# Kernel tuning notes

Hardware: AMD Instinct MI355X
Metric: run time of the kernel (lower is better)

The kernel has to match this reference:

```python
import jax, jax.numpy as jnp
import numpy as np

TOP_K = 2
NEG_INF = -1e30


def setup_inputs() -> dict:
    key = jax.random.key(0)
    ks = jax.random.split(key, 9)
    S, B, D, H, E, O = 2, 2048, 1024, 2048, 8, 1024
    return {
        "xs": jax.random.normal(ks[0], (S, B, D), jnp.float32),
        "Wg": jax.random.normal(ks[1], (D, E), jnp.float32),
        "b": jax.random.normal(ks[2], (E,), jnp.float32),
        "fc1_w": jax.random.normal(ks[3], (E, H, D), jnp.float32) * 0.02,
        "fc1_b": jax.random.normal(ks[4], (E, H), jnp.float32) * 0.02,
        "fc2_w": jax.random.normal(ks[5], (E, H, H), jnp.float32) * 0.02,
        "fc2_b": jax.random.normal(ks[6], (E, H), jnp.float32) * 0.02,
        "final_w": jax.random.normal(ks[7], (O, H), jnp.float32) * 0.02,
        "final_b": jax.random.normal(ks[8], (O,), jnp.float32) * 0.02,
    }


def reference(xs, Wg, b, fc1_w, fc1_b, fc2_w, fc2_b, final_w, final_b):
    # xs: [S, B, D] stacked x_list
    S = xs.shape[0]
    # gate logits H: [S, B, E]
    Hg = jnp.einsum('sbd,de->sbe', xs, Wg) + b
    expert_probs = jax.nn.softmax(Hg, axis=-1)  # per-view full softmax
    # top-k threshold mask (H >= kth largest value)
    topk_vals = jax.lax.top_k(Hg, TOP_K)[0]          # [S, B, K]
    thr = topk_vals[..., -1:]                         # [S, B, 1]
    H_masked = jnp.where(Hg >= thr, Hg, NEG_INF)
    G = jax.nn.softmax(H_masked, axis=-1)             # [S, B, E]
    # dense all-expert FFN: [S, B, E, H]
    h = jnp.einsum('sbd,ehd->sbeh', xs, fc1_w) + fc1_b
    h = jax.nn.relu(h)
    eo = jnp.einsum('sbeh,egh->sbeg', h, fc2_w) + fc2_b
    # gated sum over experts, averaged over views: [B, H]
    combined = jnp.einsum('sbe,sbeh->bh', G, eo) / S
    out = combined @ final_w.T + final_b               # [B, O]
    return out, expert_probs
```

## Files before the change

### kernel.cpp

```cpp
#include <hip/hip_runtime.h>
#include <stdint.h>

#define S_DIM 2
#define B_DIM 2048
#define D_DIM 1024
#define H_DIM 2048
#define E_DIM 8
#define O_DIM 1024
#define NTOK 4096
#define CAP 12288

typedef __attribute__((ext_vector_type(8))) short bf16x8;
typedef __attribute__((ext_vector_type(4))) float f32x4;

__device__ __forceinline__ unsigned short f2bf(float f) {
    union { float f; uint32_t i; } c; c.f = f;
    uint32_t r = c.i + 0x7FFFu + ((c.i >> 16) & 1u);
    return (unsigned short)(r >> 16);
}
__device__ __forceinline__ float bf2f(unsigned short u) {
    union { uint32_t i; float f; } c; c.i = (uint32_t)u << 16;
    return c.f;
}
__device__ __forceinline__ uint32_t pack2(float a, float b) {
    return (uint32_t)f2bf(a) | ((uint32_t)f2bf(b) << 16);
}
__device__ __forceinline__ void stage8(const float* __restrict__ src,
                                       unsigned short* __restrict__ dst) {
    float4 f0 = *(const float4*)src;
    float4 f1 = *(const float4*)(src + 4);
    int4 v;
    v.x = (int)pack2(f0.x, f0.y);
    v.y = (int)pack2(f0.z, f0.w);
    v.z = (int)pack2(f1.x, f1.y);
    v.w = (int)pack2(f1.z, f1.w);
    *(int4*)dst = v;
}

__device__ __forceinline__ void glds16(const unsigned short* g, unsigned short* l) {
    __builtin_amdgcn_global_load_lds(
        (__attribute__((address_space(1))) void*)g,
        (__attribute__((address_space(3))) void*)l,
        16, 0, 0);
}

__global__ __launch_bounds__(256) void convert_kernel(
    const float* __restrict__ src, unsigned short* __restrict__ dst, int n8)
{
    int i = blockIdx.x * blockDim.x + threadIdx.x;
    if (i < n8) stage8(src + (size_t)i * 8, dst + (size_t)i * 8);
}

__global__ __launch_bounds__(256) void gating_kernel(
    const float* __restrict__ xs,
    const float* __restrict__ Wg,
    const float* __restrict__ bvec,
    float* __restrict__ probs_out,
    int* __restrict__ counts,
    int* __restrict__ sel_cnt,
    int* __restrict__ sel_e,
    float* __restrict__ sel_g,
    unsigned short* __restrict__ xs_bf)
{
    const int wave = threadIdx.x >> 6;
    const int lane = threadIdx.x & 63;
    const int t = blockIdx.x * 4 + wave;
    const float* x = xs + (size_t)t * D_DIM;

    float acc[8];
#pragma unroll
    for (int e = 0; e < 8; ++e) acc[e] = 0.f;

#pragma unroll
    for (int i = 0; i < D_DIM / 64; ++i) {
        int d = i * 64 + lane;
        float xv = x[d];
        xs_bf[(size_t)t * D_DIM + d] = f2bf(xv);
        float4 w0 = *(const float4*)(Wg + (size_t)d * 8);
        float4 w1 = *(const float4*)(Wg + (size_t)d * 8 + 4);
        acc[0] += xv * w0.x; acc[1] += xv * w0.y;
        acc[2] += xv * w0.z; acc[3] += xv * w0.w;
        acc[4] += xv * w1.x; acc[5] += xv * w1.y;
        acc[6] += xv * w1.z; acc[7] += xv * w1.w;
    }
#pragma unroll
    for (int off = 32; off > 0; off >>= 1) {
#pragma unroll
        for (int e = 0; e < 8; ++e)
            acc[e] += __shfl_down(acc[e], off);
    }

    if (lane == 0) {
        float Hg[8];
#pragma unroll
        for (int e = 0; e < 8; ++e) Hg[e] = acc[e] + bvec[e];

        int a1 = 0;
#pragma unroll
        for (int e = 1; e < 8; ++e) if (Hg[e] > Hg[a1]) a1 = e;
        float m1 = Hg[a1];
        float m2 = -1e30f;
#pragma unroll
        for (int e = 0; e < 8; ++e) if (e != a1 && Hg[e] > m2) m2 = Hg[e];

        float ex[8]; float sum = 0.f;
#pragma unroll
        for (int e = 0; e < 8; ++e) { ex[e] = expf(Hg[e] - m1); sum += ex[e]; }
        float inv = 1.f / sum;
#pragma unroll
        for (int e = 0; e < 8; ++e)
            probs_out[(size_t)t * 8 + e] = ex[e] * inv;

        float den = 0.f;
#pragma unroll
        for (int e = 0; e < 8; ++e) if (Hg[e] >= m2) den += ex[e];
        float invd = 1.f / den;
        int n = 0;
#pragma unroll
        for (int e = 0; e < 8; ++e) {
            if (Hg[e] >= m2) {
                sel_e[t * 8 + n] = e;
                sel_g[t * 8 + n] = ex[e] * invd;
                ++n;
                atomicAdd(&counts[e], 1);
            }
        }
        sel_cnt[t] = n;
    }
}

__global__ void scan_kernel(const int* __restrict__ counts, int* __restrict__ offsets)
{
    if (threadIdx.x == 0) {
        int tot = 0;
#pragma unroll
        for (int e = 0; e < 8; ++e) { offsets[e] = tot; tot += counts[e]; }
    }
}

__global__ __launch_bounds__(256) void scatter_kernel(
    const int* __restrict__ sel_cnt,
    const int* __restrict__ sel_e,
    const float* __restrict__ sel_g,
    const int* __restrict__ offsets,
    int* __restrict__ cursors,
    int* __restrict__ pair_token,
    float* __restrict__ pair_gate,
    int* __restrict__ tok_slot)
{
    int t = blockIdx.x * blockDim.x + threadIdx.x;
    if (t >= NTOK) return;
    int n = sel_cnt[t];
    for (int i = 0; i < n && i < 8; ++i) {
        int e = sel_e[t * 8 + i];
        int r = atomicAdd(&cursors[e], 1);
        int slot = offsets[e] + r;
        if (slot < CAP) {
            pair_token[slot] = t;
            pair_gate[slot]  = sel_g[t * 8 + i];
            tok_slot[t * 8 + i] = slot;
        } else {
            tok_slot[t * 8 + i] = -1;
        }
    }
}

__global__ __launch_bounds__(256) void fc1_kernel(
    const unsigned short* __restrict__ xs_bf,
    const unsigned short* __restrict__ fc1_wb,
    const float* __restrict__ fc1_b,
    const int* __restrict__ counts,
    const int* __restrict__ offsets,
    const int* __restrict__ pair_token,
    unsigned short* __restrict__ h)
{
    const int wg = blockIdx.x;
    const int e = wg & 7;
    const int idx = wg >> 3;
    const int mtile = idx >> 4;
    const int ntile = idx & 15;
    const int cnt = counts[e];
    if (mtile * 128 >= cnt) return;
    const int offs = offsets[e];

    __shared__ __align__(16) unsigned short As[128 * 64];
    __shared__ __align__(16) unsigned short Bs[128 * 64];

    const int tid  = threadIdx.x;
    const int lane = tid & 63;
    const int wave = tid >> 6;
    const int wr = wave >> 1, wc = wave & 1;
    const int lrow = lane & 15;
    const int kq   = lane >> 4;

    const unsigned short* aSrc[4];
    const unsigned short* bSrc[4];
    int dstOff[4];
#pragma unroll
    for (int i = 0; i < 4; ++i) {
        int c = i * 256 + tid;
        int row = c >> 3;
        int gran = (c & 7) ^ (row & 7);
        int m = mtile * 128 + row;
        int mc = m < cnt ? m : cnt - 1;
        int tok = pair_token[offs + mc];
        aSrc[i] = xs_bf + (size_t)tok * D_DIM + gran * 8;
        int n = ntile * 128 + row;
        bSrc[i] = fc1_wb + ((size_t)e * H_DIM + n) * D_DIM + gran * 8;
        dstOff[i] = (i * 256 + wave * 64) * 8;
    }

    f32x4 acc[4][4];
#pragma unroll
    for (int i = 0; i < 4; ++i)
#pragma unroll
        for (int j = 0; j < 4; ++j)
            acc[i][j] = (f32x4){0.f, 0.f, 0.f, 0.f};

    for (int k0 = 0; k0 < D_DIM; k0 += 64) {
        __syncthreads();
#pragma unroll
        for (int i = 0; i < 4; ++i) {
            glds16(aSrc[i] + k0, &As[dstOff[i]]);
            glds16(bSrc[i] + k0, &Bs[dstOff[i]]);
        }
        __syncthreads();
#pragma unroll
        for (int ks = 0; ks < 2; ++ks) {
            bf16x8 af[4], bfr[4];
            const int gr = ks * 4 + kq;
            const int sg = (gr ^ (lrow & 7)) * 8;
#pragma unroll
            for (int i = 0; i < 4; ++i) {
                af[i]  = *(const bf16x8*)&As[(wr * 64 + i * 16 + lrow) * 64 + sg];
                bfr[i] = *(const bf16x8*)&Bs[(wc * 64 + i * 16 + lrow) * 64 + sg];
            }
#pragma unroll
            for (int i = 0; i < 4; ++i)
#pragma unroll
                for (int j = 0; j < 4; ++j)
                    acc[i][j] = __builtin_amdgcn_mfma_f32_16x16x32_bf16(af[i], bfr[j], acc[i][j], 0, 0, 0);
        }
    }

    int ncol[4]; float bias[4];
#pragma unroll
    for (int j = 0; j < 4; ++j) {
        ncol[j] = ntile * 128 + wc * 64 + j * 16 + lrow;
        bias[j] = fc1_b[e * H_DIM + ncol[j]];
    }
#pragma unroll
    for (int i = 0; i < 4; ++i) {
#pragma unroll
        for (int r = 0; r < 4; ++r) {
            int m = mtile * 128 + wr * 64 + i * 16 + kq * 4 + r;
            if (m < cnt) {
                size_t base = (size_t)(offs + m) * H_DIM;
#pragma unroll
                for (int j = 0; j < 4; ++j) {
                    float v = acc[i][j][r] + bias[j];
                    h[base + ncol[j]] = f2bf(v > 0.f ? v : 0.f);
                }
            }
        }
    }
}

__global__ __launch_bounds__(256) void fc2_kernel(
    const unsigned short* __restrict__ h,
    const unsigned short* __restrict__ fc2_wb,
    const float* __restrict__ fc2_b,
    const int* __restrict__ counts,
    const int* __restrict__ offsets,
    const float* __restrict__ pair_gate,
    unsigned short* __restrict__ eo_bf)
{
    const int wg = blockIdx.x;
    const int e = wg & 7;
    const int idx = wg >> 3;
    const int mtile = idx >> 4;
    const int ntile = idx & 15;
    const int cnt = counts[e];
    if (mtile * 128 >= cnt) return;
    const int offs = offsets[e];

    __shared__ __align__(16) unsigned short As[128 * 64];
    __shared__ __align__(16) unsigned short Bs[128 * 64];

    const int tid  = threadIdx.x;
    const int lane = tid & 63;
    const int wave = tid >> 6;
    const int wr = wave >> 1, wc = wave & 1;
    const int lrow = lane & 15;
    const int kq   = lane >> 4;

    const unsigned short* aSrc[4];
    const unsigned short* bSrc[4];
    int dstOff[4];
#pragma unroll
    for (int i = 0; i < 4; ++i) {
        int c = i * 256 + tid;
        int row = c >> 3;
        int gran = (c & 7) ^ (row & 7);
        int m = mtile * 128 + row;
        int mc = m < cnt ? m : cnt - 1;
        aSrc[i] = h + (size_t)(offs + mc) * H_DIM + gran * 8;
        int n = ntile * 128 + row;
        bSrc[i] = fc2_wb + ((size_t)e * H_DIM + n) * H_DIM + gran * 8;
        dstOff[i] = (i * 256 + wave * 64) * 8;
    }

    f32x4 acc[4][4];
#pragma unroll
    for (int i = 0; i < 4; ++i)
#pragma unroll
        for (int j = 0; j < 4; ++j)
            acc[i][j] = (f32x4){0.f, 0.f, 0.f, 0.f};

    for (int k0 = 0; k0 < H_DIM; k0 += 64) {
        __syncthreads();
#pragma unroll
        for (int i = 0; i < 4; ++i) {
            glds16(aSrc[i] + k0, &As[dstOff[i]]);
            glds16(bSrc[i] + k0, &Bs[dstOff[i]]);
        }
        __syncthreads();
#pragma unroll
        for (int ks = 0; ks < 2; ++ks) {
            bf16x8 af[4], bfr[4];
            const int gr = ks * 4 + kq;
            const int sg = (gr ^ (lrow & 7)) * 8;
#pragma unroll
            for (int i = 0; i < 4; ++i) {
                af[i]  = *(const bf16x8*)&As[(wr * 64 + i * 16 + lrow) * 64 + sg];
                bfr[i] = *(const bf16x8*)&Bs[(wc * 64 + i * 16 + lrow) * 64 + sg];
            }
#pragma unroll
            for (int i = 0; i < 4; ++i)
#pragma unroll
                for (int j = 0; j < 4; ++j)
                    acc[i][j] = __builtin_amdgcn_mfma_f32_16x16x32_bf16(af[i], bfr[j], acc[i][j], 0, 0, 0);
        }
    }

    int ncol[4]; float bias[4];
#pragma unroll
    for (int j = 0; j < 4; ++j) {
        ncol[j] = ntile * 128 + wc * 64 + j * 16 + lrow;
        bias[j] = fc2_b[e * H_DIM + ncol[j]];
    }
#pragma unroll
    for (int i = 0; i < 4; ++i) {
#pragma unroll
        for (int r = 0; r < 4; ++r) {
            int m = mtile * 128 + wr * 64 + i * 16 + kq * 4 + r;
            if (m < cnt) {
                int slot = offs + m;
                float g  = pair_gate[slot] * 0.5f;
                size_t base = (size_t)slot * H_DIM;
#pragma unroll
                for (int j = 0; j < 4; ++j) {
                    float v = (acc[i][j][r] + bias[j]) * g;
                    eo_bf[base + ncol[j]] = f2bf(v);
                }
            }
        }
    }
}

__global__ __launch_bounds__(256) void reduce_kernel(
    const int* __restrict__ sel_cnt,
    const int* __restrict__ tok_slot,
    const unsigned short* __restrict__ eo_bf,
    unsigned short* __restrict__ combined_bf)
{
    const int b = blockIdx.x;
    const int h0 = threadIdx.x * 8;

    float acc[8];
#pragma unroll
    for (int j = 0; j < 8; ++j) acc[j] = 0.f;

#pragma unroll
    for (int s = 0; s < S_DIM; ++s) {
        int t = s * B_DIM + b;
        int n = sel_cnt[t];
        for (int i = 0; i < n && i < 8; ++i) {
            int slot = tok_slot[t * 8 + i];
            if (slot < 0) continue;
            bf16x8 v = *(const bf16x8*)&eo_bf[(size_t)slot * H_DIM + h0];
#pragma unroll
            for (int j = 0; j < 8; ++j)
                acc[j] += bf2f((unsigned short)v[j]);
        }
    }

    int4 o;
    o.x = (int)pack2(acc[0], acc[1]);
    o.y = (int)pack2(acc[2], acc[3]);
    o.z = (int)pack2(acc[4], acc[5]);
    o.w = (int)pack2(acc[6], acc[7]);
    *(int4*)&combined_bf[(size_t)b * H_DIM + h0] = o;
}

__global__ __launch_bounds__(256) void final_kernel(
    const unsigned short* __restrict__ combined_bf,
    const unsigned short* __restrict__ final_wb,
    const float* __restrict__ final_b,
    float* __restrict__ out)
{
    const int mtile = blockIdx.y;
    const int ntile = blockIdx.x;

    __shared__ __align__(16) unsigned short As[128 * 64];
    __shared__ __align__(16) unsigned short Bs[128 * 64];

    const int tid  = threadIdx.x;
    const int lane = tid & 63;
    const int wave = tid >> 6;
    const int wr = wave >> 1, wc = wave & 1;
    const int lrow = lane & 15;
    const int kq   = lane >> 4;

    const unsigned short* aSrc[4];
    const unsigned short* bSrc[4];
    int dstOff[4];
#pragma unroll
    for (int i = 0; i < 4; ++i) {
        int c = i * 256 + tid;
        int row = c >> 3;
        int gran = (c & 7) ^ (row & 7);
        int m = mtile * 128 + row;
        aSrc[i] = combined_bf + (size_t)m * H_DIM + gran * 8;
        int n = ntile * 128 + row;
        bSrc[i] = final_wb + (size_t)n * H_DIM + gran * 8;
        dstOff[i] = (i * 256 + wave * 64) * 8;
    }

    f32x4 acc[4][4];
#pragma unroll
    for (int i = 0; i < 4; ++i)
#pragma unroll
        for (int j = 0; j < 4; ++j)
            acc[i][j] = (f32x4){0.f, 0.f, 0.f, 0.f};

    for (int k0 = 0; k0 < H_DIM; k0 += 64) {
        __syncthreads();
#pragma unroll
        for (int i = 0; i < 4; ++i) {
            glds16(aSrc[i] + k0, &As[dstOff[i]]);
            glds16(bSrc[i] + k0, &Bs[dstOff[i]]);
        }
        __syncthreads();
#pragma unroll
        for (int ks = 0; ks < 2; ++ks) {
            bf16x8 af[4], bfr[4];
            const int gr = ks * 4 + kq;
            const int sg = (gr ^ (lrow & 7)) * 8;
#pragma unroll
            for (int i = 0; i < 4; ++i) {
                af[i]  = *(const bf16x8*)&As[(wr * 64 + i * 16 + lrow) * 64 + sg];
                bfr[i] = *(const bf16x8*)&Bs[(wc * 64 + i * 16 + lrow) * 64 + sg];
            }
#pragma unroll
            for (int i = 0; i < 4; ++i)
#pragma unroll
                for (int j = 0; j < 4; ++j)
                    acc[i][j] = __builtin_amdgcn_mfma_f32_16x16x32_bf16(af[i], bfr[j], acc[i][j], 0, 0, 0);
        }
    }

    int ncol[4]; float bias[4];
#pragma unroll
    for (int j = 0; j < 4; ++j) {
        ncol[j] = ntile * 128 + wc * 64 + j * 16 + lrow;
        bias[j] = final_b[ncol[j]];
    }
#pragma unroll
    for (int i = 0; i < 4; ++i) {
#pragma unroll
        for (int r = 0; r < 4; ++r) {
            int m = mtile * 128 + wr * 64 + i * 16 + kq * 4 + r;
#pragma unroll
            for (int j = 0; j < 4; ++j)
                out[(size_t)m * O_DIM + ncol[j]] = acc[i][j][r] + bias[j];
        }
    }
}

extern "C" void kernel_launch(void* const* d_in, const int* in_sizes, int n_in,
                              void* d_out, int out_size, void* d_ws, size_t ws_size,
                              hipStream_t stream) {
    const float* xs      = (const float*)d_in[0];
    const float* Wg      = (const float*)d_in[1];
    const float* bvec    = (const float*)d_in[2];
    const float* fc1_w   = (const float*)d_in[3];
    const float* fc1_b   = (const float*)d_in[4];
    const float* fc2_w   = (const float*)d_in[5];
    const float* fc2_b   = (const float*)d_in[6];
    const float* final_w = (const float*)d_in[7];
    const float* final_b = (const float*)d_in[8];

    float* out = (float*)d_out;
    float* probs_out = out + (size_t)B_DIM * O_DIM;

    uint8_t* w = (uint8_t*)d_ws;
    int*   counts     = (int*)(w + 0);
    int*   cursors    = (int*)(w + 64);
    int*   offsets    = (int*)(w + 128);
    int*   sel_cnt    = (int*)(w + 256);
    int*   sel_e      = (int*)(w + 0x5000);
    float* sel_g      = (float*)(w + 0x25000);
    int*   pair_token = (int*)(w + 0x45000);
    float* pair_gate  = (float*)(w + 0x51000);
    int*   tok_slot   = (int*)(w + 0x5D000);
    unsigned short* h = (unsigned short*)(w + 0x1060000);
    unsigned short* xs_bf   = (unsigned short*)(w + 0x4060000);
    unsigned short* fc1_wb  = (unsigned short*)(w + 0x4860000);
    unsigned short* fc2_wb  = (unsigned short*)(w + 0x6860000);
    unsigned short* final_wb    = (unsigned short*)(w + 0xA860000);
    unsigned short* combined_bf = (unsigned short*)(w + 0xAC60000);
    unsigned short* eo_bf       = (unsigned short*)(w + 0xB460000);

    hipMemsetAsync(w, 0, 256, stream);

    convert_kernel<<<(E_DIM * H_DIM * D_DIM / 8) / 256, 256, 0, stream>>>(
        fc1_w, fc1_wb, E_DIM * H_DIM * D_DIM / 8);
    convert_kernel<<<(E_DIM * H_DIM * H_DIM / 8) / 256, 256, 0, stream>>>(
        fc2_w, fc2_wb, E_DIM * H_DIM * H_DIM / 8);
    convert_kernel<<<(O_DIM * H_DIM / 8) / 256, 256, 0, stream>>>(
        final_w, final_wb, O_DIM * H_DIM / 8);

    gating_kernel<<<NTOK / 4, 256, 0, stream>>>(xs, Wg, bvec, probs_out,
                                                counts, sel_cnt, sel_e, sel_g, xs_bf);
    scan_kernel<<<1, 64, 0, stream>>>(counts, offsets);
    scatter_kernel<<<NTOK / 256, 256, 0, stream>>>(sel_cnt, sel_e, sel_g, offsets,
                                                   cursors, pair_token, pair_gate,
                                                   tok_slot);
    fc1_kernel<<<E_DIM * (NTOK / 128) * (H_DIM / 128), 256, 0, stream>>>(
        xs_bf, fc1_wb, fc1_b, counts, offsets, pair_token, h);
    fc2_kernel<<<E_DIM * (NTOK / 128) * (H_DIM / 128), 256, 0, stream>>>(
        h, fc2_wb, fc2_b, counts, offsets, pair_gate, eo_bf);
    reduce_kernel<<<B_DIM, 256, 0, stream>>>(sel_cnt, tok_slot, eo_bf, combined_bf);
    final_kernel<<<dim3(O_DIM / 128, B_DIM / 128), 256, 0, stream>>>(
        combined_bf, final_wb, final_b, out);
}
```

Before: 625.9 us.

## Use 256x256 double-buffered 8-wave MFMA tiles with async prefetch in expert GEMMs

Both expert GEMM kernels (fc1, fc2) now use 512-thread blocks computing 256x256 output tiles instead of 256-thread 128x128 tiles. Shared memory is double-buffered, so the next K-tile's global-to-LDS loads are issued while the current tile's MFMAs run. Each K-tile is split into four sub-phases separated by raw s_barrier calls, with s_setprio raised around the MFMA bursts. The goal is to hide memory latency and get more reuse per loaded tile. The cost is about 128KB of LDS per block, which limits occupancy, plus coarser tiles that waste more work on partial per-expert row counts.

```diff
diff --git a/kernel.cpp b/kernel.cpp
--- a/kernel.cpp
+++ b/kernel.cpp
@@ -165,7 +165,52 @@
     }
 }
 
-__global__ __launch_bounds__(256) void fc1_kernel(
+#define MFMA_PHASE(BUF, MG, NG, DOSTAGE, K0N, DODRAIN)                          \
+    {                                                                           \
+        bf16x8 af[4][2], bfr[2][2];                                             \
+        _Pragma("unroll")                                                       \
+        for (int x = 0; x < 4; ++x)                                             \
+            _Pragma("unroll")                                                   \
+            for (int ks = 0; ks < 2; ++ks)                                      \
+                af[x][ks] = *(const bf16x8*)&As[BUF][aBase + ((MG)*4 + x) * 1024 \
+                                                 + ((ks * 4 + kq) ^ swz) * 8];  \
+        _Pragma("unroll")                                                       \
+        for (int y = 0; y < 2; ++y)                                             \
+            _Pragma("unroll")                                                   \
+            for (int ks = 0; ks < 2; ++ks)                                      \
+                bfr[y][ks] = *(const bf16x8*)&Bs[BUF][bBase + ((NG)*2 + y) * 1024\
+                                                  + ((ks * 4 + kq) ^ swz) * 8]; \
+        if (DOSTAGE) {                                                          \
+            _Pragma("unroll")                                                   \
+            for (int i = 0; i < 4; ++i) {                                       \
+                glds16(aSrc[i] + (K0N), &As[(BUF) ^ 1][dstOff[i]]);             \
+                glds16(bSrc[i] + (K0N), &Bs[(BUF) ^ 1][dstOff[i]]);             \
+            }                                                                   \
+        }                                                                       \
+        __builtin_amdgcn_s_barrier();                                           \
+        __builtin_amdgcn_s_setprio(1);                                          \
+        _Pragma("unroll")                                                       \
+        for (int x = 0; x < 4; ++x)                                             \
+            _Pragma("unroll")                                                   \
+            for (int y = 0; y < 2; ++y)                                         \
+                _Pragma("unroll")                                               \
+                for (int ks = 0; ks < 2; ++ks)                                  \
+                    acc[(MG)*4 + x][(NG)*2 + y] =                               \
+                        __builtin_amdgcn_mfma_f32_16x16x32_bf16(                \
+                            af[x][ks], bfr[y][ks], acc[(MG)*4 + x][(NG)*2 + y], \
+                            0, 0, 0);                                           \
+        __builtin_amdgcn_s_setprio(0);                                          \
+        if (DODRAIN) asm volatile("s_waitcnt vmcnt(0)" ::: "memory");           \
+        __builtin_amdgcn_s_barrier();                                           \
+    }
+
+#define KTILE(BUF, DOSTAGE, K0N)                    \
+    MFMA_PHASE(BUF, 0, 0, DOSTAGE, K0N, false)      \
+    MFMA_PHASE(BUF, 0, 1, false,   0,   false)      \
+    MFMA_PHASE(BUF, 1, 0, false,   0,   false)      \
+    MFMA_PHASE(BUF, 1, 1, false,   0,   DOSTAGE)
+
+__global__ __launch_bounds__(512, 2) void fc1_kernel(
     const unsigned short* __restrict__ xs_bf,
     const unsigned short* __restrict__ fc1_wb,
     const float* __restrict__ fc1_b,
@@ -177,83 +222,78 @@
     const int wg = blockIdx.x;
     const int e = wg & 7;
     const int idx = wg >> 3;
-    const int mtile = idx >> 4;
-    const int ntile = idx & 15;
+    const int mtile = idx >> 3;
+    const int ntile = idx & 7;
     const int cnt = counts[e];
-    if (mtile * 128 >= cnt) return;
+    if (mtile * 256 >= cnt) return;
     const int offs = offsets[e];
 
-    __shared__ __align__(16) unsigned short As[128 * 64];
-    __shared__ __align__(16) unsigned short Bs[128 * 64];
+    __shared__ __align__(16) unsigned short As[2][256 * 64];
+    __shared__ __align__(16) unsigned short Bs[2][256 * 64];
 
     const int tid  = threadIdx.x;
     const int lane = tid & 63;
-    const int wave = tid >> 6;
-    const int wr = wave >> 1, wc = wave & 1;
+    const int wid  = tid >> 6;
+    const int wr   = wid >> 2;
+    const int wcn  = wid & 3;
     const int lrow = lane & 15;
     const int kq   = lane >> 4;
+    const int swz  = lrow & 7;
+    const int aBase = (wr * 128 + lrow) * 64;
+    const int bBase = (wcn * 64 + lrow) * 64;
 
     const unsigned short* aSrc[4];
     const unsigned short* bSrc[4];
     int dstOff[4];
 #pragma unroll
     for (int i = 0; i < 4; ++i) {
-        int c = i * 256 + tid;
+        int c = i * 512 + tid;
         int row = c >> 3;
         int gran = (c & 7) ^ (row & 7);
-        int m = mtile * 128 + row;
+        int m = mtile * 256 + row;
         int mc = m < cnt ? m : cnt - 1;
         int tok = pair_token[offs + mc];
         aSrc[i] = xs_bf + (size_t)tok * D_DIM + gran * 8;
-        int n = ntile * 128 + row;
+        int n = ntile * 256 + row;
         bSrc[i] = fc1_wb + ((size_t)e * H_DIM + n) * D_DIM + gran * 8;
-        dstOff[i] = (i * 256 + wave * 64) * 8;
-    }
-
-    f32x4 acc[4][4];
-#pragma unroll
-    for (int i = 0; i < 4; ++i)
+        dstOff[i] = (i * 512 + wid * 64) * 8;
+    }
+
+    f32x4 acc[8][4];
+#pragma unroll
+    for (int i = 0; i < 8; ++i)
 #pragma unroll
         for (int j = 0; j < 4; ++j)
             acc[i][j] = (f32x4){0.f, 0.f, 0.f, 0.f};
 
-    for (int k0 = 0; k0 < D_DIM; k0 += 64) {
-        __syncthreads();
-#pragma unroll
-        for (int i = 0; i < 4; ++i) {
-            glds16(aSrc[i] + k0, &As[dstOff[i]]);
-            glds16(bSrc[i] + k0, &Bs[dstOff[i]]);
-        }
-        __syncthreads();
-#pragma unroll
-        for (int ks = 0; ks < 2; ++ks) {
-            bf16x8 af[4], bfr[4];
-            const int gr = ks * 4 + kq;
-            const int sg = (gr ^ (lrow & 7)) * 8;
-#pragma unroll
-            for (int i = 0; i < 4; ++i) {
-                af[i]  = *(const bf16x8*)&As[(wr * 64 + i * 16 + lrow) * 64 + sg];
-                bfr[i] = *(const bf16x8*)&Bs[(wc * 64 + i * 16 + lrow) * 64 + sg];
-            }
-#pragma unroll
-            for (int i = 0; i < 4; ++i)
-#pragma unroll
-                for (int j = 0; j < 4; ++j)
-                    acc[i][j] = __builtin_amdgcn_mfma_f32_16x16x32_bf16(af[i], bfr[j], acc[i][j], 0, 0, 0);
-        }
+#pragma unroll
+    for (int i = 0; i < 4; ++i) {
+        glds16(aSrc[i], &As[0][dstOff[i]]);
+        glds16(bSrc[i], &Bs[0][dstOff[i]]);
+    }
+    asm volatile("s_waitcnt vmcnt(0)" ::: "memory");
+    __builtin_amdgcn_s_barrier();
+
+    const int NT = D_DIM / 64;
+    for (int t = 0; t < NT; t += 2) {
+        const int k1 = (t + 1) * 64;
+        const int k2 = (t + 2) * 64;
+        const bool s2 = (t + 2) < NT;
+        KTILE(0, true, k1)
+        KTILE(1, s2, k2)
     }
 
     int ncol[4]; float bias[4];
 #pragma unroll
     for (int j = 0; j < 4; ++j) {
-        ncol[j] = ntile * 128 + wc * 64 + j * 16 + lrow;
+        ncol[j] = ntile * 256 + wcn * 64 + j * 16 + lrow;
         bias[j] = fc1_b[e * H_DIM + ncol[j]];
     }
 #pragma unroll
-    for (int i = 0; i < 4; ++i) {
+    for (int i = 0; i < 8; ++i) {
 #pragma unroll
         for (int r = 0; r < 4; ++r) {
-            int m = mtile * 128 + wr * 64 + i * 16 + kq * 4 + r;
+            int m = mtile * 256 + wr * 128 + i * 16 + kq * 4 + r;
             if (m < cnt) {
                 size_t base = (size_t)(offs + m) * H_DIM;
 #pragma unroll
@@ -266,7 +306,7 @@
     }
 }
 
-__global__ __launch_bounds__(256) void fc2_kernel(
+__global__ __launch_bounds__(512, 2) void fc2_kernel(
     const unsigned short* __restrict__ h,
     const unsigned short* __restrict__ fc2_wb,
     const float* __restrict__ fc2_b,
@@ -278,82 +318,77 @@
     const int wg = blockIdx.x;
     const int e = wg & 7;
     const int idx = wg >> 3;
-    const int mtile = idx >> 4;
-    const int ntile = idx & 15;
+    const int mtile = idx >> 3;
+    const int ntile = idx & 7;
     const int cnt = counts[e];
-    if (mtile * 128 >= cnt) return;
+    if (mtile * 256 >= cnt) return;
     const int offs = offsets[e];
 
-    __shared__ __align__(16) unsigned short As[128 * 64];
-    __shared__ __align__(16) unsigned short Bs[128 * 64];
+    __shared__ __align__(16) unsigned short As[2][256 * 64];
+    __shared__ __align__(16) unsigned short Bs[2][256 * 64];
 
     const int tid  = threadIdx.x;
     const int lane = tid & 63;
-    const int wave = tid >> 6;
-    const int wr = wave >> 1, wc = wave & 1;
+    const int wid  = tid >> 6;
+    const int wr   = wid >> 2;
+    const int wcn  = wid & 3;
     const int lrow = lane & 15;
     const int kq   = lane >> 4;
+    const int swz  = lrow & 7;
+    const int aBase = (wr * 128 + lrow) * 64;
+    const int bBase = (wcn * 64 + lrow) * 64;
 
     const unsigned short* aSrc[4];
     const unsigned short* bSrc[4];
     int dstOff[4];
 #pragma unroll
     for (int i = 0; i < 4; ++i) {
-        int c = i * 256 + tid;
+        int c = i * 512 + tid;
         int row = c >> 3;
         int gran = (c & 7) ^ (row & 7);
-        int m = mtile * 128 + row;
+        int m = mtile * 256 + row;
         int mc = m < cnt ? m : cnt - 1;
         aSrc[i] = h + (size_t)(offs + mc) * H_DIM + gran * 8;
-        int n = ntile * 128 + row;
+        int n = ntile * 256 + row;
         bSrc[i] = fc2_wb + ((size_t)e * H_DIM + n) * H_DIM + gran * 8;
-        dstOff[i] = (i * 256 + wave * 64) * 8;
-    }
-
-    f32x4 acc[4][4];
-#pragma unroll
-    for (int i = 0; i < 4; ++i)
+        dstOff[i] = (i * 512 + wid * 64) * 8;
+    }
+
+    f32x4 acc[8][4];
+#pragma unroll
+    for (int i = 0; i < 8; ++i)
 #pragma unroll
         for (int j = 0; j < 4; ++j)
             acc[i][j] = (f32x4){0.f, 0.f, 0.f, 0.f};
 
-    for (int k0 = 0; k0 < H_DIM; k0 += 64) {
-        __syncthreads();
-#pragma unroll
-        for (int i = 0; i < 4; ++i) {
-            glds16(aSrc[i] + k0, &As[dstOff[i]]);
-            glds16(bSrc[i] + k0, &Bs[dstOff[i]]);
-        }
-        __syncthreads();
-#pragma unroll
-        for (int ks = 0; ks < 2; ++ks) {
-            bf16x8 af[4], bfr[4];
-            const int gr = ks * 4 + kq;
-            const int sg = (gr ^ (lrow & 7)) * 8;
-#pragma unroll
-            for (int i = 0; i < 4; ++i) {
-                af[i]  = *(const bf16x8*)&As[(wr * 64 + i * 16 + lrow) * 64 + sg];
-                bfr[i] = *(const bf16x8*)&Bs[(wc * 64 + i * 16 + lrow) * 64 + sg];
-            }
-#pragma unroll
-            for (int i = 0; i < 4; ++i)
-#pragma unroll
-                for (int j = 0; j < 4; ++j)
-                    acc[i][j] = __builtin_amdgcn_mfma_f32_16x16x32_bf16(af[i], bfr[j], acc[i][j], 0, 0, 0);
-        }
+#pragma unroll
+    for (int i = 0; i < 4; ++i) {
+        glds16(aSrc[i], &As[0][dstOff[i]]);
+        glds16(bSrc[i], &Bs[0][dstOff[i]]);
+    }
+    asm volatile("s_waitcnt vmcnt(0)" ::: "memory");
+    __builtin_amdgcn_s_barrier();
+
+    const int NT = H_DIM / 64;
+    for (int t = 0; t < NT; t += 2) {
+        const int k1 = (t + 1) * 64;
+        const int k2 = (t + 2) * 64;
+        const bool s2 = (t + 2) < NT;
+        KTILE(0, true, k1)
+        KTILE(1, s2, k2)
     }
 
     int ncol[4]; float bias[4];
 #pragma unroll
     for (int j = 0; j < 4; ++j) {
-        ncol[j] = ntile * 128 + wc * 64 + j * 16 + lrow;
+        ncol[j] = ntile * 256 + wcn * 64 + j * 16 + lrow;
         bias[j] = fc2_b[e * H_DIM + ncol[j]];
     }
 #pragma unroll
-    for (int i = 0; i < 4; ++i) {
+    for (int i = 0; i < 8; ++i) {
 #pragma unroll
         for (int r = 0; r < 4; ++r) {
-            int m = mtile * 128 + wr * 64 + i * 16 + kq * 4 + r;
+            int m = mtile * 256 + wr * 128 + i * 16 + kq * 4 + r;
             if (m < cnt) {
                 int slot = offs + m;
                 float g  = pair_gate[slot] * 0.5f;
@@ -537,9 +572,9 @@
     scatter_kernel<<<NTOK / 256, 256, 0, stream>>>(sel_cnt, sel_e, sel_g, offsets,
                                                    cursors, pair_token, pair_gate,
                                                    tok_slot);
-    fc1_kernel<<<E_DIM * (NTOK / 128) * (H_DIM / 128), 256, 0, stream>>>(
+    fc1_kernel<<<E_DIM * (NTOK / 256) * (H_DIM / 256), 512, 0, stream>>>(
         xs_bf, fc1_wb, fc1_b, counts, offsets, pair_token, h);
-    fc2_kernel<<<E_DIM * (NTOK / 128) * (H_DIM / 128), 256, 0, stream>>>(
+    fc2_kernel<<<E_DIM * (NTOK / 256) * (H_DIM / 256), 512, 0, stream>>>(
         h, fc2_wb, fc2_b, counts, offsets, pair_gate, eo_bf);
     reduce_kernel<<<B_DIM, 256, 0, stream>>>(sel_cnt, tok_slot, eo_bf, combined_bf);
     final_kernel<<<dim3(O_DIM / 128, B_DIM / 128), 256, 0, stream>>>(
```

Result: slower. 702.0 us (+12.2%).

## Enlarge expert GEMM tiles to 128x256 with 8x4 MFMA per wave

Applied to the files above, without the earlier changes.

The fc1 and fc2 expert GEMM kernels now use a 128x256 output tile instead of 128x128. Each wave computes all 128 rows against its own 64 columns, giving an 8x4 block of MFMA accumulators, and B tile staging in shared memory is doubled. The grid is halved to match, and launch bounds ask for two workgroups per CU. The aim is more arithmetic per LDS and global load and fewer redundant activation loads, at the cost of higher register and LDS use per block and fewer blocks to fill the GPU.

```diff
diff --git a/kernel.cpp b/kernel.cpp
--- a/kernel.cpp
+++ b/kernel.cpp
@@ -165,7 +165,8 @@
     }
 }
 
-__global__ __launch_bounds__(256) void fc1_kernel(
+
+__global__ __launch_bounds__(256, 2) void fc1_kernel(
     const unsigned short* __restrict__ xs_bf,
     const unsigned short* __restrict__ fc1_wb,
     const float* __restrict__ fc1_b,
@@ -177,25 +178,24 @@
     const int wg = blockIdx.x;
     const int e = wg & 7;
     const int idx = wg >> 3;
-    const int mtile = idx >> 4;
-    const int ntile = idx & 15;
+    const int mtile = idx >> 3;
+    const int ntile = idx & 7;
     const int cnt = counts[e];
     if (mtile * 128 >= cnt) return;
     const int offs = offsets[e];
 
     __shared__ __align__(16) unsigned short As[128 * 64];
-    __shared__ __align__(16) unsigned short Bs[128 * 64];
+    __shared__ __align__(16) unsigned short Bs[256 * 64];
 
     const int tid  = threadIdx.x;
     const int lane = tid & 63;
-    const int wave = tid >> 6;
-    const int wr = wave >> 1, wc = wave & 1;
+    const int wid  = tid >> 6;
     const int lrow = lane & 15;
     const int kq   = lane >> 4;
+    const int swz  = lrow & 7;
 
     const unsigned short* aSrc[4];
-    const unsigned short* bSrc[4];
-    int dstOff[4];
+    int aDst[4];
 #pragma unroll
     for (int i = 0; i < 4; ++i) {
         int c = i * 256 + tid;
@@ -205,14 +205,23 @@
         int mc = m < cnt ? m : cnt - 1;
         int tok = pair_token[offs + mc];
         aSrc[i] = xs_bf + (size_t)tok * D_DIM + gran * 8;
-        int n = ntile * 128 + row;
+        aDst[i] = (i * 256 + wid * 64) * 8;
+    }
+    const unsigned short* bSrc[8];
+    int bDst[8];
+#pragma unroll
+    for (int i = 0; i < 8; ++i) {
+        int c = i * 256 + tid;
+        int row = c >> 3;
+        int gran = (c & 7) ^ (row & 7);
+        int n = ntile * 256 + row;
         bSrc[i] = fc1_wb + ((size_t)e * H_DIM + n) * D_DIM + gran * 8;
-        dstOff[i] = (i * 256 + wave * 64) * 8;
-    }
-
-    f32x4 acc[4][4];
-#pragma unroll
-    for (int i = 0; i < 4; ++i)
+        bDst[i] = (i * 256 + wid * 64) * 8;
+    }
+
+    f32x4 acc[8][4];
+#pragma unroll
+    for (int i = 0; i < 8; ++i)
 #pragma unroll
         for (int j = 0; j < 4; ++j)
             acc[i][j] = (f32x4){0.f, 0.f, 0.f, 0.f};
@@ -220,40 +229,40 @@
     for (int k0 = 0; k0 < D_DIM; k0 += 64) {
         __syncthreads();
 #pragma unroll
-        for (int i = 0; i < 4; ++i) {
-            glds16(aSrc[i] + k0, &As[dstOff[i]]);
-            glds16(bSrc[i] + k0, &Bs[dstOff[i]]);
-        }
+        for (int i = 0; i < 4; ++i) glds16(aSrc[i] + k0, &As[aDst[i]]);
+#pragma unroll
+        for (int i = 0; i < 8; ++i) glds16(bSrc[i] + k0, &Bs[bDst[i]]);
         __syncthreads();
 #pragma unroll
         for (int ks = 0; ks < 2; ++ks) {
-            bf16x8 af[4], bfr[4];
-            const int gr = ks * 4 + kq;
-            const int sg = (gr ^ (lrow & 7)) * 8;
-#pragma unroll
-            for (int i = 0; i < 4; ++i) {
-                af[i]  = *(const bf16x8*)&As[(wr * 64 + i * 16 + lrow) * 64 + sg];
-                bfr[i] = *(const bf16x8*)&Bs[(wc * 64 + i * 16 + lrow) * 64 + sg];
-            }
-#pragma unroll
-            for (int i = 0; i < 4; ++i)
+            const int sg = ((ks * 4 + kq) ^ swz) * 8;
+            bf16x8 af[8], bfr[4];
+#pragma unroll
+            for (int i = 0; i < 8; ++i)
+                af[i] = *(const bf16x8*)&As[(i * 16 + lrow) * 64 + sg];
+#pragma unroll
+            for (int j = 0; j < 4; ++j)
+                bfr[j] = *(const bf16x8*)&Bs[(wid * 64 + j * 16 + lrow) * 64 + sg];
+#pragma unroll
+            for (int i = 0; i < 8; ++i)
 #pragma unroll
                 for (int j = 0; j < 4; ++j)
-                    acc[i][j] = __builtin_amdgcn_mfma_f32_16x16x32_bf16(af[i], bfr[j], acc[i][j], 0, 0, 0);
+                    acc[i][j] = __builtin_amdgcn_mfma_f32_16x16x32_bf16(
+                        af[i], bfr[j], acc[i][j], 0, 0, 0);
         }
     }
 
     int ncol[4]; float bias[4];
 #pragma unroll
     for (int j = 0; j < 4; ++j) {
-        ncol[j] = ntile * 128 + wc * 64 + j * 16 + lrow;
+        ncol[j] = ntile * 256 + wid * 64 + j * 16 + lrow;
         bias[j] = fc1_b[e * H_DIM + ncol[j]];
     }
 #pragma unroll
-    for (int i = 0; i < 4; ++i) {
+    for (int i = 0; i < 8; ++i) {
 #pragma unroll
         for (int r = 0; r < 4; ++r) {
-            int m = mtile * 128 + wr * 64 + i * 16 + kq * 4 + r;
+            int m = mtile * 128 + i * 16 + kq * 4 + r;
             if (m < cnt) {
                 size_t base = (size_t)(offs + m) * H_DIM;
 #pragma unroll
@@ -266,7 +275,7 @@
     }
 }
 
-__global__ __launch_bounds__(256) void fc2_kernel(
+__global__ __launch_bounds__(256, 2) void fc2_kernel(
     const unsigned short* __restrict__ h,
     const unsigned short* __restrict__ fc2_wb,
     const float* __restrict__ fc2_b,
@@ -278,25 +287,24 @@
     const int wg = blockIdx.x;
     const int e = wg & 7;
     const int idx = wg >> 3;
-    const int mtile = idx >> 4;
-    const int ntile = idx & 15;
+    const int mtile = idx >> 3;
+    const int ntile = idx & 7;
     const int cnt = counts[e];
     if (mtile * 128 >= cnt) return;
     const int offs = offsets[e];
 
     __shared__ __align__(16) unsigned short As[128 * 64];
-    __shared__ __align__(16) unsigned short Bs[128 * 64];
+    __shared__ __align__(16) unsigned short Bs[256 * 64];
 
     const int tid  = threadIdx.x;
     const int lane = tid & 63;
-    const int wave = tid >> 6;
-    const int wr = wave >> 1, wc = wave & 1;
+    const int wid  = tid >> 6;
     const int lrow = lane & 15;
     const int kq   = lane >> 4;
+    const int swz  = lrow & 7;
 
     const unsigned short* aSrc[4];
-    const unsigned short* bSrc[4];
-    int dstOff[4];
+    int aDst[4];
 #pragma unroll
     for (int i = 0; i < 4; ++i) {
         int c = i * 256 + tid;
@@ -305,14 +313,23 @@
         int m = mtile * 128 + row;
         int mc = m < cnt ? m : cnt - 1;
         aSrc[i] = h + (size_t)(offs + mc) * H_DIM + gran * 8;
-        int n = ntile * 128 + row;
+        aDst[i] = (i * 256 + wid * 64) * 8;
+    }
+    const unsigned short* bSrc[8];
+    int bDst[8];
+#pragma unroll
+    for (int i = 0; i < 8; ++i) {
+        int c = i * 256 + tid;
+        int row = c >> 3;
+        int gran = (c & 7) ^ (row & 7);
+        int n = ntile * 256 + row;
         bSrc[i] = fc2_wb + ((size_t)e * H_DIM + n) * H_DIM + gran * 8;
-        dstOff[i] = (i * 256 + wave * 64) * 8;
-    }
-
-    f32x4 acc[4][4];
-#pragma unroll
-    for (int i = 0; i < 4; ++i)
+        bDst[i] = (i * 256 + wid * 64) * 8;
+    }
+
+    f32x4 acc[8][4];
+#pragma unroll
+    for (int i = 0; i < 8; ++i)
 #pragma unroll
         for (int j = 0; j < 4; ++j)
             acc[i][j] = (f32x4){0.f, 0.f, 0.f, 0.f};
@@ -320,40 +337,40 @@
     for (int k0 = 0; k0 < H_DIM; k0 += 64) {
         __syncthreads();
 #pragma unroll
-        for (int i = 0; i < 4; ++i) {
-            glds16(aSrc[i] + k0, &As[dstOff[i]]);
-            glds16(bSrc[i] + k0, &Bs[dstOff[i]]);
-        }
+        for (int i = 0; i < 4; ++i) glds16(aSrc[i] + k0, &As[aDst[i]]);
+#pragma unroll
+        for (int i = 0; i < 8; ++i) glds16(bSrc[i] + k0, &Bs[bDst[i]]);
         __syncthreads();
 #pragma unroll
         for (int ks = 0; ks < 2; ++ks) {
-            bf16x8 af[4], bfr[4];
-            const int gr = ks * 4 + kq;
-            const int sg = (gr ^ (lrow & 7)) * 8;
-#pragma unroll
-            for (int i = 0; i < 4; ++i) {
-                af[i]  = *(const bf16x8*)&As[(wr * 64 + i * 16 + lrow) * 64 + sg];
-                bfr[i] = *(const bf16x8*)&Bs[(wc * 64 + i * 16 + lrow) * 64 + sg];
-            }
-#pragma unroll
-            for (int i = 0; i < 4; ++i)
+            const int sg = ((ks * 4 + kq) ^ swz) * 8;
+            bf16x8 af[8], bfr[4];
+#pragma unroll
+            for (int i = 0; i < 8; ++i)
+                af[i] = *(const bf16x8*)&As[(i * 16 + lrow) * 64 + sg];
+#pragma unroll
+            for (int j = 0; j < 4; ++j)
+                bfr[j] = *(const bf16x8*)&Bs[(wid * 64 + j * 16 + lrow) * 64 + sg];
+#pragma unroll
+            for (int i = 0; i < 8; ++i)
 #pragma unroll
                 for (int j = 0; j < 4; ++j)
-                    acc[i][j] = __builtin_amdgcn_mfma_f32_16x16x32_bf16(af[i], bfr[j], acc[i][j], 0, 0, 0);
+                    acc[i][j] = __builtin_amdgcn_mfma_f32_16x16x32_bf16(
+                        af[i], bfr[j], acc[i][j], 0, 0, 0);
         }
     }
 
     int ncol[4]; float bias[4];
 #pragma unroll
     for (int j = 0; j < 4; ++j) {
-        ncol[j] = ntile * 128 + wc * 64 + j * 16 + lrow;
+        ncol[j] = ntile * 256 + wid * 64 + j * 16 + lrow;
         bias[j] = fc2_b[e * H_DIM + ncol[j]];
     }
 #pragma unroll
-    for (int i = 0; i < 4; ++i) {
+    for (int i = 0; i < 8; ++i) {
 #pragma unroll
         for (int r = 0; r < 4; ++r) {
-            int m = mtile * 128 + wr * 64 + i * 16 + kq * 4 + r;
+            int m = mtile * 128 + i * 16 + kq * 4 + r;
             if (m < cnt) {
                 int slot = offs + m;
                 float g  = pair_gate[slot] * 0.5f;
@@ -537,9 +554,9 @@
     scatter_kernel<<<NTOK / 256, 256, 0, stream>>>(sel_cnt, sel_e, sel_g, offsets,
                                                    cursors, pair_token, pair_gate,
                                                    tok_slot);
-    fc1_kernel<<<E_DIM * (NTOK / 128) * (H_DIM / 128), 256, 0, stream>>>(
+    fc1_kernel<<<E_DIM * (NTOK / 128) * (H_DIM / 256), 256, 0, stream>>>(
         xs_bf, fc1_wb, fc1_b, counts, offsets, pair_token, h);
-    fc2_kernel<<<E_DIM * (NTOK / 128) * (H_DIM / 128), 256, 0, stream>>>(
+    fc2_kernel<<<E_DIM * (NTOK / 128) * (H_DIM / 256), 256, 0, stream>>>(
         h, fc2_wb, fc2_b, counts, offsets, pair_gate, eo_bf);
     reduce_kernel<<<B_DIM, 256, 0, stream>>>(sel_cnt, tok_slot, eo_bf, combined_bf);
     final_kernel<<<dim3(O_DIM / 128, B_DIM / 128), 256, 0, stream>>>(
```

New measurement: 638.4 us. About the same (+2.0%).
